# Performance work log

Measured on AMD Instinct MI355X. Metric: run time of the kernel, lower is better.

The kernel has to match this reference:

```python
import jax, jax.numpy as jnp
import numpy as np

HIDDEN = 2048
NUM_HEADS = 16
HEAD_DIM = HIDDEN // NUM_HEADS
BATCH, SEQ = 2, 2048


def setup_inputs() -> dict:
    key = jax.random.key(0)
    ks = jax.random.split(key, 9)
    s = 1.0 / np.sqrt(HIDDEN)
    return {
        "hidden_state": jax.random.normal(ks[0], (BATCH, SEQ, HIDDEN), dtype=jnp.float32),
        "Wq": jax.random.normal(ks[1], (HIDDEN, HIDDEN), dtype=jnp.float32) * s,
        "bq": jax.random.normal(ks[2], (HIDDEN,), dtype=jnp.float32) * 0.01,
        "Wk": jax.random.normal(ks[3], (HIDDEN, HIDDEN), dtype=jnp.float32) * s,
        "bk": jax.random.normal(ks[4], (HIDDEN,), dtype=jnp.float32) * 0.01,
        "Wv": jax.random.normal(ks[5], (HIDDEN, HIDDEN), dtype=jnp.float32) * s,
        "bv": jax.random.normal(ks[6], (HIDDEN,), dtype=jnp.float32) * 0.01,
        "Wo": jax.random.normal(ks[7], (HIDDEN, HIDDEN), dtype=jnp.float32) * s,
        "bo": jax.random.normal(ks[8], (HIDDEN,), dtype=jnp.float32) * 0.01,
    }


def _split_heads(x):
    # (B, S, H*D) -> (B, H, S, D)
    b, s, _ = x.shape
    return x.reshape(b, s, NUM_HEADS, HEAD_DIM).transpose(0, 2, 1, 3)


def reference(hidden_state, Wq, bq, Wk, bk, Wv, bv, Wo, bo):
    q = _split_heads(hidden_state @ Wq + bq)
    k = _split_heads(hidden_state @ Wk + bk)
    v = _split_heads(hidden_state @ Wv + bv)
    scale = 1.0 / jnp.sqrt(jnp.asarray(HEAD_DIM, dtype=hidden_state.dtype))
    scores = jnp.einsum("bhqd,bhkd->bhqk", q, k) * scale  # (B,H,S,S)
    probs = jax.nn.softmax(scores, axis=-1)
    out = jnp.einsum("bhqk,bhkd->bhqd", probs, v)  # (B,H,S,D)
    b, h, s, d = out.shape
    out = out.transpose(0, 2, 1, 3).reshape(b, s, h * d)  # merge heads
    return out @ Wo + bo
```

## Files before the change

### kernel.cpp

```cpp
#include <hip/hip_runtime.h>
#include <math.h>

typedef __bf16 bf16;
typedef __bf16 bf16x4 __attribute__((ext_vector_type(4)));
typedef __bf16 bf16x8 __attribute__((ext_vector_type(8)));
typedef float  f32x4  __attribute__((ext_vector_type(4)));

#define HIDDEN 2048
#define NH     16
#define HD     128
#define BATCH  2
#define SEQ    2048
#define MROWS  (BATCH*SEQ)
#define NQKV   (3*HIDDEN)

__device__ __forceinline__ void async16(const bf16* g, bf16* l) {
  __builtin_amdgcn_global_load_lds(
      (const __attribute__((address_space(1))) void*)g,
      (__attribute__((address_space(3))) void*)l, 16, 0, 0);
}

__global__ __launch_bounds__(256) void cast_f32_bf16_kernel(
    const float* __restrict__ src, bf16* __restrict__ dst, int n4) {
  int i = blockIdx.x * 256 + threadIdx.x;
  if (i >= n4) return;
  float4 f = ((const float4*)src)[i];
  bf16x4 o;
  o[0] = (bf16)f.x; o[1] = (bf16)f.y; o[2] = (bf16)f.z; o[3] = (bf16)f.w;
  ((bf16x4*)dst)[i] = o;
}

__global__ __launch_bounds__(256) void transpose_cast4_kernel(
    const float* __restrict__ s0, const float* __restrict__ s1,
    const float* __restrict__ s2, const float* __restrict__ s3,
    bf16* __restrict__ d0, bf16* __restrict__ d1,
    bf16* __restrict__ d2, bf16* __restrict__ d3) {
  const float* src; bf16* dst;
  switch (blockIdx.z) {
    case 0: src = s0; dst = d0; break;
    case 1: src = s1; dst = d1; break;
    case 2: src = s2; dst = d2; break;
    default: src = s3; dst = d3; break;
  }
  __shared__ float t[32][33];
  int x  = blockIdx.x * 32 + threadIdx.x;
  int y0 = blockIdx.y * 32;
#pragma unroll
  for (int i = 0; i < 32; i += 8)
    t[threadIdx.y + i][threadIdx.x] = src[(size_t)(y0 + threadIdx.y + i) * HIDDEN + x];
  __syncthreads();
  int xo  = blockIdx.y * 32 + threadIdx.x;
  int yo0 = blockIdx.x * 32;
#pragma unroll
  for (int i = 0; i < 32; i += 8)
    dst[(size_t)(yo0 + threadIdx.y + i) * HIDDEN + xo] = (bf16)t[threadIdx.x][threadIdx.y + i];
}

__global__ __launch_bounds__(256) void concat3_kernel(
    const float* __restrict__ a, const float* __restrict__ b,
    const float* __restrict__ c, float* __restrict__ dst) {
  int i = blockIdx.x * 256 + threadIdx.x;
  float v = (i < 2048) ? a[i] : (i < 4096 ? b[i - 2048] : c[i - 4096]);
  dst[i] = v;
}

__global__ __launch_bounds__(256) void transpose_v_kernel(
    const bf16* __restrict__ QKV, bf16* __restrict__ Vt) {
  __shared__ bf16 t[32][33];
  int bh = blockIdx.z, b = bh >> 4, h = bh & 15;
  const bf16* src = QKV + (size_t)b * SEQ * NQKV + 2 * HIDDEN + h * HD;
  bf16* dst = Vt + (size_t)bh * HD * SEQ;
  int s0 = blockIdx.x * 32, d0 = blockIdx.y * 32;
#pragma unroll
  for (int i = 0; i < 32; i += 8)
    t[threadIdx.y + i][threadIdx.x] = src[(size_t)(s0 + threadIdx.y + i) * NQKV + d0 + threadIdx.x];
  __syncthreads();
#pragma unroll
  for (int i = 0; i < 32; i += 8)
    dst[(size_t)(d0 + threadIdx.y + i) * SEQ + s0 + threadIdx.x] = t[threadIdx.x][threadIdx.y + i];
}

template <typename OutT>
__global__ __launch_bounds__(256) void gemm_bt_bias(
    const bf16* __restrict__ A, const bf16* __restrict__ Bt,
    const float* __restrict__ bias, OutT* __restrict__ C, int N, int K) {
  __shared__ bf16 Ash[128 * 64];
  __shared__ bf16 Bsh[128 * 64];
  const int tid = threadIdx.x;
  const int wave = tid >> 6, lane = tid & 63, quad = lane >> 4, l16 = lane & 15;
  const int wm = (wave & 1) * 64, wn = (wave >> 1) * 64;
  const int m0 = blockIdx.x * 128, n0 = blockIdx.y * 128;

  const f32x4 zero4 = {0.f, 0.f, 0.f, 0.f};
  f32x4 acc[4][4];
#pragma unroll
  for (int i = 0; i < 4; i++)
#pragma unroll
    for (int j = 0; j < 4; j++) acc[i][j] = zero4;

  const int crow = tid >> 3, ccc = tid & 7;
  const int cd = (ccc - crow) & 7;
  const int l7 = l16 & 7;

  const bf16* pa[4];
  const bf16* pb[4];
#pragma unroll
  for (int s = 0; s < 4; s++) {
    pa[s] = &A[(size_t)(m0 + s * 32 + crow) * K + cd * 8];
    pb[s] = &Bt[(size_t)(n0 + s * 32 + crow) * K + cd * 8];
  }

  for (int kt = 0; kt < K; kt += 64) {
    __syncthreads();
#pragma unroll
    for (int s = 0; s < 4; s++) {
      async16(pa[s], &Ash[s * 2048 + tid * 8]);
      async16(pb[s], &Bsh[s * 2048 + tid * 8]);
      pa[s] += 64; pb[s] += 64;
    }
    __syncthreads();

#pragma unroll
    for (int kk = 0; kk < 2; kk++) {
      const int pc = (kk * 4 + quad + l7) & 7;
      bf16x8 af[4], bfr[4];
#pragma unroll
      for (int i = 0; i < 4; i++) af[i]  = *(const bf16x8*)&Ash[(wm + i * 16 + l16) * 64 + pc * 8];
#pragma unroll
      for (int j = 0; j < 4; j++) bfr[j] = *(const bf16x8*)&Bsh[(wn + j * 16 + l16) * 64 + pc * 8];
#pragma unroll
      for (int i = 0; i < 4; i++)
#pragma unroll
        for (int j = 0; j < 4; j++)
          acc[i][j] = __builtin_amdgcn_mfma_f32_16x16x32_bf16(af[i], bfr[j], acc[i][j], 0, 0, 0);
    }
  }

#pragma unroll
  for (int i = 0; i < 4; i++)
#pragma unroll
    for (int j = 0; j < 4; j++) {
      int n = n0 + wn + j * 16 + l16;
      float bv = bias[n];
#pragma unroll
      for (int r = 0; r < 4; r++) {
        int m = m0 + wm + i * 16 + quad * 4 + r;
        C[(size_t)m * N + n] = (OutT)(acc[i][j][r] + bv);
      }
    }
}

#define KTS   64
#define PPAD  72

__global__ __launch_bounds__(256, 2) void flash_attn_kernel(
    const bf16* __restrict__ QKV, const bf16* __restrict__ Vt, bf16* __restrict__ O) {
  const int bh = blockIdx.y, b = bh >> 4, h = bh & 15;
  const int q0 = blockIdx.x * 128;
  const int tid = threadIdx.x, wave = tid >> 6, lane = tid & 63, quad = lane >> 4, l16 = lane & 15;

  const bf16* Qb  = QKV + (size_t)b * SEQ * NQKV + h * HD;
  const bf16* Kb  = QKV + (size_t)b * SEQ * NQKV + HIDDEN + h * HD;
  const bf16* Vtb = Vt + (size_t)bh * HD * SEQ;

  __shared__ bf16 Ksh[KTS * HD];
  __shared__ bf16 Vsh[HD * KTS];
  __shared__ bf16 Psh[128 * PPAD];

  const int qrow = q0 + wave * 32;
  const float sc = 0.08838834764831845f * 1.44269504088896340f;

  bf16x8 qf[2][4];
#pragma unroll
  for (int mt = 0; mt < 2; mt++)
#pragma unroll
    for (int kk = 0; kk < 4; kk++) {
      bf16x8 t = *(const bf16x8*)&Qb[(size_t)(qrow + mt * 16 + l16) * NQKV + kk * 32 + quad * 8];
#pragma unroll
      for (int j = 0; j < 8; j++) t[j] = (bf16)((float)t[j] * sc);
      qf[mt][kk] = t;
    }

  const f32x4 zero4 = {0.f, 0.f, 0.f, 0.f};
  f32x4 oacc[2][8];
#pragma unroll
  for (int mt = 0; mt < 2; mt++)
#pragma unroll
    for (int nt = 0; nt < 8; nt++) oacc[mt][nt] = zero4;

  float lrun[2] = {0.f, 0.f};

  const int krp = tid >> 4, kpp = tid & 15;
  const int vrp = tid >> 3, vpp = tid & 7;
  const int l7 = l16 & 7;

  const bf16* pk[4];
  const bf16* pv[4];
#pragma unroll
  for (int s = 0; s < 4; s++) {
    int r  = s * 16 + krp;
    pk[s] = &Kb[(size_t)r * NQKV + (kpp ^ (r & 7)) * 8];
    int rv = s * 32 + vrp;
    pv[s] = &Vtb[(size_t)rv * SEQ + (vpp ^ (rv & 7)) * 8];
  }

  for (int kt = 0; kt < SEQ; kt += KTS) {
    __syncthreads();
#pragma unroll
    for (int s = 0; s < 4; s++) {
      async16(pk[s], &Ksh[s * 2048 + tid * 8]);
      async16(pv[s], &Vsh[s * 2048 + tid * 8]);
      pk[s] += (size_t)KTS * NQKV;
      pv[s] += KTS;
    }
    __syncthreads();

    f32x4 st[2][4];
#pragma unroll
    for (int mt = 0; mt < 2; mt++)
#pragma unroll
      for (int nt = 0; nt < 4; nt++) st[mt][nt] = zero4;
#pragma unroll
    for (int kk = 0; kk < 4; kk++) {
      const int p = (4 * kk + quad) ^ l7;
      bf16x8 kf[4];
#pragma unroll
      for (int nt = 0; nt < 4; nt++)
        kf[nt] = *(const bf16x8*)&Ksh[(nt * 16 + l16) * HD + p * 8];
#pragma unroll
      for (int mt = 0; mt < 2; mt++)
#pragma unroll
        for (int nt = 0; nt < 4; nt++)
          st[mt][nt] = __builtin_amdgcn_mfma_f32_16x16x32_bf16(kf[nt], qf[mt][kk], st[mt][nt], 0, 0, 0);
    }

    float rs[2] = {0.f, 0.f};
#pragma unroll
    for (int mt = 0; mt < 2; mt++)
#pragma unroll
      for (int nt = 0; nt < 4; nt++) {
        bf16x4 pk4;
#pragma unroll
        for (int r = 0; r < 4; r++) {
          float p = exp2f(st[mt][nt][r]);
          rs[mt] += p;
          pk4[r] = (bf16)p;
        }
        *(bf16x4*)&Psh[(wave * 32 + mt * 16 + l16) * PPAD + nt * 16 + quad * 4] = pk4;
      }
#pragma unroll
    for (int mt = 0; mt < 2; mt++) {
      float t = rs[mt];
      t += __shfl_xor(t, 16);
      t += __shfl_xor(t, 32);
      lrun[mt] += t;
    }

#pragma unroll
    for (int kk2 = 0; kk2 < 2; kk2++) {
      bf16x8 pf[2], vf[8];
#pragma unroll
      for (int mt = 0; mt < 2; mt++)
        pf[mt] = *(const bf16x8*)&Psh[(wave * 32 + mt * 16 + l16) * PPAD + kk2 * 32 + quad * 8];
#pragma unroll
      for (int nt = 0; nt < 8; nt++) {
        int p = (4 * kk2 + quad) ^ l7;
        vf[nt] = *(const bf16x8*)&Vsh[(nt * 16 + l16) * KTS + p * 8];
      }
#pragma unroll
      for (int mt = 0; mt < 2; mt++)
#pragma unroll
        for (int nt = 0; nt < 8; nt++)
          oacc[mt][nt] = __builtin_amdgcn_mfma_f32_16x16x32_bf16(pf[mt], vf[nt], oacc[mt][nt], 0, 0, 0);
    }
  }

#pragma unroll
  for (int mt = 0; mt < 2; mt++) {
    float inv[4];
#pragma unroll
    for (int r = 0; r < 4; r++)
      inv[r] = 1.0f / __shfl(lrun[mt], (lane & 48) | (quad * 4 + r));
#pragma unroll
    for (int nt = 0; nt < 8; nt++)
#pragma unroll
      for (int r = 0; r < 4; r++) {
        int q = qrow + mt * 16 + quad * 4 + r;
        int d = nt * 16 + l16;
        O[(size_t)(b * SEQ + q) * HIDDEN + h * HD + d] = (bf16)(oacc[mt][nt][r] * inv[r]);
      }
  }
}

extern "C" void kernel_launch(void* const* d_in, const int* in_sizes, int n_in,
                              void* d_out, int out_size, void* d_ws, size_t ws_size,
                              hipStream_t stream) {
  const float* hs = (const float*)d_in[0];
  const float* Wq = (const float*)d_in[1];
  const float* bq = (const float*)d_in[2];
  const float* Wk = (const float*)d_in[3];
  const float* bk = (const float*)d_in[4];
  const float* Wv = (const float*)d_in[5];
  const float* bv = (const float*)d_in[6];
  const float* Wo = (const float*)d_in[7];
  const float* bo = (const float*)d_in[8];
  float* out = (float*)d_out;

  char* ws = (char*)d_ws;
  bf16*  Abf   = (bf16*)(ws);
  bf16*  WtQKV = (bf16*)(ws + 16777216);
  bf16*  WtO   = (bf16*)(ws + 41943040);
  float* biasQ = (float*)(ws + 50331648);
  bf16*  QKV   = (bf16*)(ws + 50356224);
  bf16*  VT    = (bf16*)(ws + 100687872);
  bf16*  Obf   = (bf16*)(ws + 117465088);

  dim3 tb(32, 8);
  cast_f32_bf16_kernel<<<8192, 256, 0, stream>>>(hs, Abf, 2097152);
  transpose_cast4_kernel<<<dim3(64, 64, 4), tb, 0, stream>>>(
      Wq, Wk, Wv, Wo,
      WtQKV, WtQKV + 2048 * 2048, WtQKV + 2 * 2048 * 2048, WtO);
  concat3_kernel<<<24, 256, 0, stream>>>(bq, bk, bv, biasQ);

  gemm_bt_bias<bf16><<<dim3(32, 48), 256, 0, stream>>>(Abf, WtQKV, biasQ, QKV, NQKV, HIDDEN);
  transpose_v_kernel<<<dim3(64, 4, 32), tb, 0, stream>>>(QKV, VT);
  flash_attn_kernel<<<dim3(16, 32), 256, 0, stream>>>(QKV, VT, Obf);
  gemm_bt_bias<float><<<dim3(32, 16), 256, 0, stream>>>(Obf, WtO, bo, out, HIDDEN, HIDDEN);
}
```

Before: 406.6 us.

## Pipeline GEMM with triple-buffered LDS, 128x256 tiles and 8 waves

Rewrites the bias GEMM to use 512 threads with 128x256 output tiles and a three-stage LDS ring, so global-to-LDS loads for tile t+2 overlap MFMA work on tile t. The k-loop is split into four quadrant phases that interleave fragment reads, prefetch issue and MFMA bursts, using s_setprio and explicit waitcnt and barriers. The aim is to hide load latency and cut redundant B loads per output element. In exchange the kernel uses much more LDS, launches half as many blocks (which may hurt occupancy and the wave count for the smaller output GEMM), and depends on hand-tuned waitcnt values that must exactly match the number of outstanding loads.

```diff
diff --git a/kernel.cpp b/kernel.cpp
--- a/kernel.cpp
+++ b/kernel.cpp
@@ -81,15 +81,16 @@
 }
 
 template <typename OutT>
-__global__ __launch_bounds__(256) void gemm_bt_bias(
+__global__ __launch_bounds__(512, 2) void gemm_bt_bias(
     const bf16* __restrict__ A, const bf16* __restrict__ Bt,
     const float* __restrict__ bias, OutT* __restrict__ C, int N, int K) {
-  __shared__ bf16 Ash[128 * 64];
-  __shared__ bf16 Bsh[128 * 64];
+  __shared__ bf16 Ash[3 * 128 * 64];
+  __shared__ bf16 Bsh[3 * 256 * 64];
+
   const int tid = threadIdx.x;
-  const int wave = tid >> 6, lane = tid & 63, quad = lane >> 4, l16 = lane & 15;
-  const int wm = (wave & 1) * 64, wn = (wave >> 1) * 64;
-  const int m0 = blockIdx.x * 128, n0 = blockIdx.y * 128;
+  const int wave = tid >> 6, lane = tid & 63, quad = lane >> 4, l16 = lane & 15, l7 = l16 & 7;
+  const int wm = (wave >> 2) * 64, wn = (wave & 3) * 64;
+  const int m0 = blockIdx.x * 128, n0 = blockIdx.y * 256;
 
   const f32x4 zero4 = {0.f, 0.f, 0.f, 0.f};
   f32x4 acc[4][4];
@@ -100,40 +101,124 @@
 
   const int crow = tid >> 3, ccc = tid & 7;
   const int cd = (ccc - crow) & 7;
-  const int l7 = l16 & 7;
-
-  const bf16* pa[4];
+
+  const bf16* pa[2];
   const bf16* pb[4];
 #pragma unroll
-  for (int s = 0; s < 4; s++) {
-    pa[s] = &A[(size_t)(m0 + s * 32 + crow) * K + cd * 8];
-    pb[s] = &Bt[(size_t)(n0 + s * 32 + crow) * K + cd * 8];
-  }
-
-  for (int kt = 0; kt < K; kt += 64) {
-    __syncthreads();
-#pragma unroll
-    for (int s = 0; s < 4; s++) {
-      async16(pa[s], &Ash[s * 2048 + tid * 8]);
-      async16(pb[s], &Bsh[s * 2048 + tid * 8]);
-      pa[s] += 64; pb[s] += 64;
-    }
-    __syncthreads();
-
-#pragma unroll
-    for (int kk = 0; kk < 2; kk++) {
-      const int pc = (kk * 4 + quad + l7) & 7;
-      bf16x8 af[4], bfr[4];
-#pragma unroll
-      for (int i = 0; i < 4; i++) af[i]  = *(const bf16x8*)&Ash[(wm + i * 16 + l16) * 64 + pc * 8];
-#pragma unroll
-      for (int j = 0; j < 4; j++) bfr[j] = *(const bf16x8*)&Bsh[(wn + j * 16 + l16) * 64 + pc * 8];
-#pragma unroll
-      for (int i = 0; i < 4; i++)
-#pragma unroll
-        for (int j = 0; j < 4; j++)
-          acc[i][j] = __builtin_amdgcn_mfma_f32_16x16x32_bf16(af[i], bfr[j], acc[i][j], 0, 0, 0);
-    }
+  for (int s = 0; s < 2; s++) pa[s] = &A[(size_t)(m0 + s * 64 + crow) * K + cd * 8];
+#pragma unroll
+  for (int s = 0; s < 4; s++) pb[s] = &Bt[(size_t)(n0 + s * 64 + crow) * K + cd * 8];
+
+  const int NT = K >> 6;
+
+#pragma unroll
+  for (int s = 0; s < 2; s++) { async16(pa[s], &Ash[0 * 8192 + s * 4096 + tid * 8]); pa[s] += 64; }
+#pragma unroll
+  for (int s = 0; s < 4; s++) { async16(pb[s], &Bsh[0 * 16384 + s * 4096 + tid * 8]); pb[s] += 64; }
+#pragma unroll
+  for (int s = 0; s < 2; s++) { async16(pa[s], &Ash[1 * 8192 + s * 4096 + tid * 8]); pa[s] += 64; }
+#pragma unroll
+  for (int s = 0; s < 4; s++) { async16(pb[s], &Bsh[1 * 16384 + s * 4096 + tid * 8]); pb[s] += 64; }
+  asm volatile("s_waitcnt vmcnt(6)" ::: "memory");
+  __builtin_amdgcn_s_barrier();
+
+  int cur = 0;
+  for (int t = 0; t < NT; ++t) {
+    const bool pf = (t + 2 < NT);
+    int nxt2 = cur + 2; if (nxt2 >= 3) nxt2 -= 3;
+    const bf16* Ac = &Ash[cur * 8192];
+    const bf16* Bc = &Bsh[cur * 16384];
+
+    bf16x8 af[4][2], bfr[4][2];
+
+#pragma unroll
+    for (int i = 0; i < 2; i++)
+#pragma unroll
+      for (int kk = 0; kk < 2; kk++)
+        af[i][kk] = *(const bf16x8*)&Ac[(wm + i * 16 + l16) * 64 + (((kk * 4 + quad) + l7) & 7) * 8];
+#pragma unroll
+    for (int j = 0; j < 2; j++)
+#pragma unroll
+      for (int kk = 0; kk < 2; kk++)
+        bfr[j][kk] = *(const bf16x8*)&Bc[(wn + j * 16 + l16) * 64 + (((kk * 4 + quad) + l7) & 7) * 8];
+    if (pf) {
+#pragma unroll
+      for (int s = 0; s < 2; s++) { async16(pa[s], &Ash[nxt2 * 8192 + s * 4096 + tid * 8]); pa[s] += 64; }
+    }
+    __builtin_amdgcn_s_barrier();
+    asm volatile("s_waitcnt lgkmcnt(0)" ::: "memory");
+    __builtin_amdgcn_sched_barrier(0);
+    __builtin_amdgcn_s_setprio(1);
+#pragma unroll
+    for (int kk = 0; kk < 2; kk++)
+#pragma unroll
+      for (int i = 0; i < 2; i++)
+#pragma unroll
+        for (int j = 0; j < 2; j++)
+          acc[i][j] = __builtin_amdgcn_mfma_f32_16x16x32_bf16(af[i][kk], bfr[j][kk], acc[i][j], 0, 0, 0);
+    __builtin_amdgcn_s_setprio(0);
+    __builtin_amdgcn_s_barrier();
+
+#pragma unroll
+    for (int j = 2; j < 4; j++)
+#pragma unroll
+      for (int kk = 0; kk < 2; kk++)
+        bfr[j][kk] = *(const bf16x8*)&Bc[(wn + j * 16 + l16) * 64 + (((kk * 4 + quad) + l7) & 7) * 8];
+    if (pf) {
+      async16(pb[0], &Bsh[nxt2 * 16384 + 0 * 4096 + tid * 8]); pb[0] += 64;
+      async16(pb[1], &Bsh[nxt2 * 16384 + 1 * 4096 + tid * 8]); pb[1] += 64;
+    }
+    __builtin_amdgcn_s_barrier();
+    asm volatile("s_waitcnt lgkmcnt(0)" ::: "memory");
+    __builtin_amdgcn_sched_barrier(0);
+    __builtin_amdgcn_s_setprio(1);
+#pragma unroll
+    for (int kk = 0; kk < 2; kk++)
+#pragma unroll
+      for (int i = 0; i < 2; i++)
+#pragma unroll
+        for (int j = 2; j < 4; j++)
+          acc[i][j] = __builtin_amdgcn_mfma_f32_16x16x32_bf16(af[i][kk], bfr[j][kk], acc[i][j], 0, 0, 0);
+    __builtin_amdgcn_s_setprio(0);
+    __builtin_amdgcn_s_barrier();
+
+#pragma unroll
+    for (int i = 2; i < 4; i++)
+#pragma unroll
+      for (int kk = 0; kk < 2; kk++)
+        af[i][kk] = *(const bf16x8*)&Ac[(wm + i * 16 + l16) * 64 + (((kk * 4 + quad) + l7) & 7) * 8];
+    if (pf) {
+      async16(pb[2], &Bsh[nxt2 * 16384 + 2 * 4096 + tid * 8]); pb[2] += 64;
+      async16(pb[3], &Bsh[nxt2 * 16384 + 3 * 4096 + tid * 8]); pb[3] += 64;
+    }
+    __builtin_amdgcn_s_barrier();
+    asm volatile("s_waitcnt lgkmcnt(0)" ::: "memory");
+    __builtin_amdgcn_sched_barrier(0);
+    __builtin_amdgcn_s_setprio(1);
+#pragma unroll
+    for (int kk = 0; kk < 2; kk++)
+#pragma unroll
+      for (int i = 2; i < 4; i++)
+#pragma unroll
+        for (int j = 2; j < 4; j++)
+          acc[i][j] = __builtin_amdgcn_mfma_f32_16x16x32_bf16(af[i][kk], bfr[j][kk], acc[i][j], 0, 0, 0);
+    __builtin_amdgcn_s_setprio(0);
+    __builtin_amdgcn_s_barrier();
+
+    __builtin_amdgcn_s_setprio(1);
+#pragma unroll
+    for (int kk = 0; kk < 2; kk++)
+#pragma unroll
+      for (int i = 2; i < 4; i++)
+#pragma unroll
+        for (int j = 0; j < 2; j++)
+          acc[i][j] = __builtin_amdgcn_mfma_f32_16x16x32_bf16(af[i][kk], bfr[j][kk], acc[i][j], 0, 0, 0);
+    __builtin_amdgcn_s_setprio(0);
+    if (pf) asm volatile("s_waitcnt vmcnt(6)" ::: "memory");
+    else    asm volatile("s_waitcnt vmcnt(0)" ::: "memory");
+    __builtin_amdgcn_s_barrier();
+
+    cur += 1; if (cur >= 3) cur -= 3;
   }
 
 #pragma unroll
@@ -322,8 +407,8 @@
       WtQKV, WtQKV + 2048 * 2048, WtQKV + 2 * 2048 * 2048, WtO);
   concat3_kernel<<<24, 256, 0, stream>>>(bq, bk, bv, biasQ);
 
-  gemm_bt_bias<bf16><<<dim3(32, 48), 256, 0, stream>>>(Abf, WtQKV, biasQ, QKV, NQKV, HIDDEN);
+  gemm_bt_bias<bf16><<<dim3(32, 24), 512, 0, stream>>>(Abf, WtQKV, biasQ, QKV, NQKV, HIDDEN);
   transpose_v_kernel<<<dim3(64, 4, 32), tb, 0, stream>>>(QKV, VT);
   flash_attn_kernel<<<dim3(16, 32), 256, 0, stream>>>(QKV, VT, Obf);
-  gemm_bt_bias<float><<<dim3(32, 16), 256, 0, stream>>>(Obf, WtO, bo, out, HIDDEN, HIDDEN);
-}
+  gemm_bt_bias<float><<<dim3(32, 8), 512, 0, stream>>>(Obf, WtO, bo, out, HIDDEN, HIDDEN);
+}
```

Result: slower. 415.2 us (+2.1%).

## Use 256x256-tile 8-wave pipelined GEMM for the QKV projection

Applied to the files above, without the earlier changes.

Adds a new GEMM kernel with 256x256 output tiles, 512 threads, and double-buffered LDS split into halves. A+B halves are streamed asynchronously, interleaved with four MFMA phases per k-step, with setprio and explicit waitcnt/barriers. It replaces the 128-tile GEMM for the fused QKV projection to raise arithmetic intensity and overlap global loads with compute. Risk: 128KB LDS and high register use limit occupancy, and the grid shrinks to 384 blocks on 256 CUs, which can leave a tail.

```diff
diff --git a/kernel.cpp b/kernel.cpp
--- a/kernel.cpp
+++ b/kernel.cpp
@@ -146,6 +146,158 @@
       for (int r = 0; r < 4; r++) {
         int m = m0 + wm + i * 16 + quad * 4 + r;
         C[(size_t)m * N + n] = (OutT)(acc[i][j][r] + bv);
+      }
+    }
+}
+
+template <typename OutT>
+__global__ __launch_bounds__(512, 2) void gemm_bt_bias_256(
+    const bf16* __restrict__ A, const bf16* __restrict__ Bt,
+    const float* __restrict__ bias, OutT* __restrict__ C, int N, int K) {
+  __shared__ bf16 Ash[2][2][128 * 64];
+  __shared__ bf16 Bsh[2][2][128 * 64];
+
+  const int tid = threadIdx.x;
+  const int wave = tid >> 6, lane = tid & 63, quad = lane >> 4, l16 = lane & 15, l7 = l16 & 7;
+  const int hA = wave >> 2;
+  const int wnq = wave & 3;
+  const int hB = wnq >> 1, rB0 = (wnq & 1) * 64;
+  const int m0 = blockIdx.x * 256, n0 = blockIdx.y * 256;
+
+  const f32x4 zero4 = {0.f, 0.f, 0.f, 0.f};
+  f32x4 acc[8][4];
+#pragma unroll
+  for (int i = 0; i < 8; i++)
+#pragma unroll
+    for (int j = 0; j < 4; j++) acc[i][j] = zero4;
+
+  const int crow = tid >> 3, ccc = tid & 7;
+  const int cd = (ccc - crow) & 7;
+
+  const bf16* gA[2][2];
+  const bf16* gB[2][2];
+#pragma unroll
+  for (int h = 0; h < 2; h++)
+#pragma unroll
+    for (int s = 0; s < 2; s++) {
+      gA[h][s] = &A[(size_t)(m0 + h * 128 + s * 64 + crow) * K + cd * 8];
+      gB[h][s] = &Bt[(size_t)(n0 + h * 128 + s * 64 + crow) * K + cd * 8];
+    }
+
+  auto stageA = [&](int buf, int h) {
+    async16(gA[h][0], &Ash[buf][h][0 * 4096 + tid * 8]); gA[h][0] += 64;
+    async16(gA[h][1], &Ash[buf][h][1 * 4096 + tid * 8]); gA[h][1] += 64;
+  };
+  auto stageB = [&](int buf, int h) {
+    async16(gB[h][0], &Bsh[buf][h][0 * 4096 + tid * 8]); gB[h][0] += 64;
+    async16(gB[h][1], &Bsh[buf][h][1 * 4096 + tid * 8]); gB[h][1] += 64;
+  };
+
+  const int NT = K >> 6;
+
+  stageA(0, 0); stageA(0, 1); stageB(0, 0); stageB(0, 1);
+  stageA(1, 0);
+  asm volatile("s_waitcnt vmcnt(2)" ::: "memory");
+  __builtin_amdgcn_s_barrier();
+
+  for (int t = 0; t < NT; ++t) {
+    const int cur = t & 1, nxt = cur ^ 1;
+    const bool s1 = (t + 1 < NT), s2 = (t + 2 < NT);
+    const bf16* Ab = Ash[cur][hA];
+    const bf16* Bb = Bsh[cur][hB];
+
+    bf16x8 af[4][2], bfr[4][2];
+
+#pragma unroll
+    for (int mi = 0; mi < 4; mi++)
+#pragma unroll
+      for (int ks = 0; ks < 2; ks++)
+        af[mi][ks] = *(const bf16x8*)&Ab[(mi * 16 + l16) * 64 + (((ks * 4 + quad) + l7) & 7) * 8];
+#pragma unroll
+    for (int ni = 0; ni < 2; ni++)
+#pragma unroll
+      for (int ks = 0; ks < 2; ks++)
+        bfr[ni][ks] = *(const bf16x8*)&Bb[(rB0 + ni * 16 + l16) * 64 + (((ks * 4 + quad) + l7) & 7) * 8];
+    if (s1) stageA(nxt, 1);
+    __builtin_amdgcn_s_barrier();
+    asm volatile("s_waitcnt lgkmcnt(0)" ::: "memory");
+    __builtin_amdgcn_sched_barrier(0);
+    __builtin_amdgcn_s_setprio(1);
+#pragma unroll
+    for (int ks = 0; ks < 2; ks++)
+#pragma unroll
+      for (int mi = 0; mi < 4; mi++)
+#pragma unroll
+        for (int ni = 0; ni < 2; ni++)
+          acc[mi][ni] = __builtin_amdgcn_mfma_f32_16x16x32_bf16(af[mi][ks], bfr[ni][ks], acc[mi][ni], 0, 0, 0);
+    __builtin_amdgcn_s_setprio(0);
+    __builtin_amdgcn_s_barrier();
+
+#pragma unroll
+    for (int ni = 2; ni < 4; ni++)
+#pragma unroll
+      for (int ks = 0; ks < 2; ks++)
+        bfr[ni][ks] = *(const bf16x8*)&Bb[(rB0 + ni * 16 + l16) * 64 + (((ks * 4 + quad) + l7) & 7) * 8];
+    if (s1) stageB(nxt, 0);
+    __builtin_amdgcn_s_barrier();
+    asm volatile("s_waitcnt lgkmcnt(0)" ::: "memory");
+    __builtin_amdgcn_sched_barrier(0);
+    __builtin_amdgcn_s_setprio(1);
+#pragma unroll
+    for (int ks = 0; ks < 2; ks++)
+#pragma unroll
+      for (int mi = 0; mi < 4; mi++)
+#pragma unroll
+        for (int ni = 2; ni < 4; ni++)
+          acc[mi][ni] = __builtin_amdgcn_mfma_f32_16x16x32_bf16(af[mi][ks], bfr[ni][ks], acc[mi][ni], 0, 0, 0);
+    __builtin_amdgcn_s_setprio(0);
+    __builtin_amdgcn_s_barrier();
+
+#pragma unroll
+    for (int mi = 0; mi < 4; mi++)
+#pragma unroll
+      for (int ks = 0; ks < 2; ks++)
+        af[mi][ks] = *(const bf16x8*)&Ab[((mi + 4) * 16 + l16) * 64 + (((ks * 4 + quad) + l7) & 7) * 8];
+    if (s1) stageB(nxt, 1);
+    __builtin_amdgcn_s_barrier();
+    asm volatile("s_waitcnt lgkmcnt(0)" ::: "memory");
+    __builtin_amdgcn_sched_barrier(0);
+    __builtin_amdgcn_s_setprio(1);
+#pragma unroll
+    for (int ks = 0; ks < 2; ks++)
+#pragma unroll
+      for (int mi = 0; mi < 4; mi++)
+#pragma unroll
+        for (int ni = 0; ni < 2; ni++)
+          acc[4 + mi][ni] = __builtin_amdgcn_mfma_f32_16x16x32_bf16(af[mi][ks], bfr[ni][ks], acc[4 + mi][ni], 0, 0, 0);
+    __builtin_amdgcn_s_setprio(0);
+    __builtin_amdgcn_s_barrier();
+
+    if (s2) stageA(cur, 0);
+    __builtin_amdgcn_s_setprio(1);
+#pragma unroll
+    for (int ks = 0; ks < 2; ks++)
+#pragma unroll
+      for (int mi = 0; mi < 4; mi++)
+#pragma unroll
+        for (int ni = 2; ni < 4; ni++)
+          acc[4 + mi][ni] = __builtin_amdgcn_mfma_f32_16x16x32_bf16(af[mi][ks], bfr[ni][ks], acc[4 + mi][ni], 0, 0, 0);
+    __builtin_amdgcn_s_setprio(0);
+    if (s2) asm volatile("s_waitcnt vmcnt(2)" ::: "memory");
+    else    asm volatile("s_waitcnt vmcnt(0)" ::: "memory");
+    __builtin_amdgcn_s_barrier();
+  }
+
+#pragma unroll
+  for (int mi = 0; mi < 8; mi++)
+#pragma unroll
+    for (int ni = 0; ni < 4; ni++) {
+      int n = n0 + wnq * 64 + ni * 16 + l16;
+      float bv = bias[n];
+#pragma unroll
+      for (int r = 0; r < 4; r++) {
+        int m = m0 + hA * 128 + mi * 16 + quad * 4 + r;
+        C[(size_t)m * N + n] = (OutT)(acc[mi][ni][r] + bv);
       }
     }
 }
@@ -322,7 +474,7 @@
       WtQKV, WtQKV + 2048 * 2048, WtQKV + 2 * 2048 * 2048, WtO);
   concat3_kernel<<<24, 256, 0, stream>>>(bq, bk, bv, biasQ);
 
-  gemm_bt_bias<bf16><<<dim3(32, 48), 256, 0, stream>>>(Abf, WtQKV, biasQ, QKV, NQKV, HIDDEN);
+  gemm_bt_bias_256<bf16><<<dim3(16, 24), 512, 0, stream>>>(Abf, WtQKV, biasQ, QKV, NQKV, HIDDEN);
   transpose_v_kernel<<<dim3(64, 4, 32), tb, 0, stream>>>(QKV, VT);
   flash_attn_kernel<<<dim3(16, 32), 256, 0, stream>>>(QKV, VT, Obf);
   gemm_bt_bias<float><<<dim3(32, 16), 256, 0, stream>>>(Obf, WtO, bo, out, HIDDEN, HIDDEN);
```

Result: no change. 409.8 us (+0.8%).
